# Kernel optimization log

Hardware: AMD Instinct MI355X
Metric: run time of the kernel (lower is better)

## Reference

```python
import jax, jax.numpy as jnp
import numpy as np

N = 50000      # nodes
E = 800000     # edges (before self-loops)
F_IN = 767     # input feature dim
HID = 256      # hidden = 8 heads * 32
NEG_SLOPE = 0.2


def setup_inputs() -> dict:
    key = jax.random.key(0)
    ks = jax.random.split(key, 10)
    x = jax.random.normal(ks[0], (N, F_IN), dtype=jnp.float32)
    edge_index = jax.random.randint(ks[1], (2, E), 0, N, dtype=jnp.int64)
    # GATConv 1: 767 -> 8 heads x 32 (concat -> 256)
    W1 = jax.random.normal(ks[2], (F_IN, HID), dtype=jnp.float32) * 0.05
    att_src1 = jax.random.normal(ks[3], (8, 32), dtype=jnp.float32) * 0.1
    att_dst1 = jax.random.normal(ks[4], (8, 32), dtype=jnp.float32) * 0.1
    b1 = jnp.zeros((HID,), dtype=jnp.float32)
    # GATConv 2: 256 -> 1 head x 10 (mean -> 10)
    W2 = jax.random.normal(ks[5], (HID, 10), dtype=jnp.float32) * 0.05
    att_src2 = jax.random.normal(ks[6], (1, 10), dtype=jnp.float32) * 0.1
    att_dst2 = jax.random.normal(ks[7], (1, 10), dtype=jnp.float32) * 0.1
    b2 = jnp.zeros((10,), dtype=jnp.float32)
    return {"x": x, "edge_index": edge_index, "W1": W1, "att_src1": att_src1,
            "att_dst1": att_dst1, "b1": b1, "W2": W2, "att_src2": att_src2,
            "att_dst2": att_dst2, "b2": b2}


def _gat_conv(x, src, dst, W, att_s, att_d, b, heads, ch, concat):
    """PyG GATConv (eval mode, dropout inactive). x:[N,Fin], src/dst:[E']."""
    n = x.shape[0]
    h = (x @ W).reshape(n, heads, ch)                      # [N,H,C]
    a_s = jnp.sum(h * att_s, axis=-1)                      # [N,H]
    a_d = jnp.sum(h * att_d, axis=-1)                      # [N,H]
    e = jax.nn.leaky_relu(a_s[src] + a_d[dst], NEG_SLOPE)  # [E',H]
    # destination-grouped (segment) softmax, numerically stable
    m = jax.lax.stop_gradient(jax.ops.segment_max(e, dst, num_segments=n))
    p = jnp.exp(e - m[dst])                                # [E',H]
    denom = jax.ops.segment_sum(p, dst, num_segments=n)    # [N,H]
    alpha = p / (denom[dst] + 1e-16)                       # [E',H]
    # scatter-aggregate weighted messages
    out = jax.ops.segment_sum(alpha[:, :, None] * h[src], dst, num_segments=n)
    out = out.reshape(n, heads * ch) if concat else out.mean(axis=1)
    return out + b


def reference(x, edge_index, W1, att_src1, att_dst1, b1, W2, att_src2, att_dst2, b2):
    n = x.shape[0]
    loops = jnp.arange(n, dtype=edge_index.dtype)
    src = jnp.concatenate([edge_index[0], loops])
    dst = jnp.concatenate([edge_index[1], loops])
    h = jax.nn.elu(_gat_conv(x, src, dst, W1, att_src1, att_dst1, b1, 8, 32, True))
    # dropout is a no-op in eval mode
    return _gat_conv(h, src, dst, W2, att_src2, att_dst2, b2, 1, 10, False)
```

## Files before the change

kernel.cpp:

```cpp
#include <hip/hip_runtime.h>
#include <hip/hip_fp16.h>

#define N_NODES 50000
#define N_EDGES 800000
#define EL (N_EDGES + N_NODES)
#define F_IN 767
#define HID 256
#define NHEAD 8
#define KSTEPS 24
#define NCH 12
#define NB_SCAN 49

typedef __attribute__((ext_vector_type(8))) short short8;
typedef __attribute__((ext_vector_type(4))) float f32x4;

struct H4 { __half2 a, b; };

static __device__ __forceinline__ unsigned short f2bf(float f) {
  unsigned int u = __float_as_uint(f);
  unsigned int r = (u + 0x7fffu + ((u >> 16) & 1u)) >> 16;
  return (unsigned short)r;
}
static __device__ __forceinline__ float bf2f(unsigned short h) {
  return __uint_as_float(((unsigned int)h) << 16);
}

__global__ __launch_bounds__(256) void prep_kernel(
    const float* __restrict__ W, short* __restrict__ Wh, short* __restrict__ Wl) {
  int idx = blockIdx.x * 256 + threadIdx.x;
  int k = idx >> 8, n = idx & 255;
  float v = (k < F_IN) ? W[k * HID + n] : 0.f;
  unsigned short h = f2bf(v);
  float lf = v - bf2f(h);
  unsigned short lo = f2bf(lf);
  int ks = k >> 5, oct = (k >> 3) & 3, j = k & 7;
  int nf = n >> 4;
  int l = (n & 15) | (oct << 4);
  int addr = ((ks * 16 + nf) * 64 + l) * 8 + j;
  Wh[addr] = (short)h;
  Wl[addr] = (short)lo;
}

__global__ __launch_bounds__(256, 2) void gemm1_mfma_kernel(
    const float* __restrict__ x, const short* __restrict__ Wh,
    const short* __restrict__ Wl, __half* __restrict__ h1h,
    const float* __restrict__ att_s, const float* __restrict__ att_d,
    float* __restrict__ as1, float* __restrict__ ad1) {
  __shared__ __align__(16) short Ah[2][2][2048];
  const int tid = threadIdx.x;
  const int lane = tid & 63, wav = tid >> 6;
  const int m0 = blockIdx.x * 64;
  const int m_local = tid >> 2, oct = tid & 3;
  const int gm = m0 + m_local;
  const bool vrow = (gm < N_NODES);
  const long xbase = (long)gm * F_IN;
  const int wu0 = ((m_local >> 4) * 64) + ((m_local & 15) | (oct << 4));
  const int wu = wu0 ^ ((((unsigned)wu0 >> 4) & 3) << 1);

  float atts[4], attd[4];
#pragma unroll
  for (int nf = 0; nf < 4; ++nf) {
    int c = wav * 64 + nf * 16 + (lane & 15);
    atts[nf] = att_s[c];
    attd[nf] = att_d[c];
  }

  f32x4 acc[4][4];
#pragma unroll
  for (int i = 0; i < 4; ++i)
#pragma unroll
    for (int j = 0; j < 4; ++j) acc[i][j] = (f32x4){0.f, 0.f, 0.f, 0.f};

  float xc[16], xn[16];
  {
    int kb = oct * 8;
    if (vrow) {
#pragma unroll
      for (int ki = 0; ki < 2; ++ki)
#pragma unroll
        for (int j = 0; j < 8; ++j) {
          xc[ki * 8 + j] = x[xbase + kb + ki * 32 + j];
          xn[ki * 8 + j] = x[xbase + 64 + kb + ki * 32 + j];
        }
    } else {
#pragma unroll
      for (int j = 0; j < 16; ++j) { xc[j] = 0.f; xn[j] = 0.f; }
    }
  }
  short8 bhc[4], blc[4];
  {
    const short* wb = Wh + ((wav * 4) * 64 + lane) * 8;
    const short* wbl = Wl + ((wav * 4) * 64 + lane) * 8;
#pragma unroll
    for (int nf = 0; nf < 4; ++nf) {
      bhc[nf] = *(const short8*)(wb + nf * 512);
      blc[nf] = *(const short8*)(wbl + nf * 512);
    }
  }

#pragma unroll 2
  for (int c = 0; c < NCH; ++c) {
#pragma unroll
    for (int ki = 0; ki < 2; ++ki) {
      short8 hi8;
#pragma unroll
      for (int j = 0; j < 8; ++j) hi8[j] = (short)f2bf(xc[ki * 8 + j]);
      *(short8*)&Ah[c & 1][ki][wu * 8] = hi8;
    }
    {
#pragma unroll
      for (int j = 0; j < 16; ++j) xc[j] = xn[j];
      int s = c + 2;
      if (s < NCH - 1) {
        int kb = s * 64 + oct * 8;
        if (vrow) {
#pragma unroll
          for (int ki = 0; ki < 2; ++ki)
#pragma unroll
            for (int j = 0; j < 8; ++j) xn[ki * 8 + j] = x[xbase + kb + ki * 32 + j];
        } else {
#pragma unroll
          for (int j = 0; j < 16; ++j) xn[j] = 0.f;
        }
      } else if (s == NCH - 1) {
        int kb = s * 64 + oct * 8;
#pragma unroll
        for (int ki = 0; ki < 2; ++ki)
#pragma unroll
          for (int j = 0; j < 8; ++j) {
            int k = kb + ki * 32 + j;
            xn[ki * 8 + j] = (vrow && k < F_IN) ? x[xbase + k] : 0.f;
          }
      }
    }
    __syncthreads();
#pragma unroll
    for (int ki = 0; ki < 2; ++ki) {
      const int ksg = c * 2 + ki;
      short8 ah[4];
#pragma unroll
      for (int mf = 0; mf < 4; ++mf) {
        int u = mf * 64 + lane;
        int us = u ^ ((((unsigned)u >> 4) & 3) << 1);
        ah[mf] = *(short8*)&Ah[c & 1][ki][us * 8];
      }
      short8 bhn[4], bln[4];
      if (ksg + 1 < KSTEPS) {
        const short* wb = Wh + (((ksg + 1) * 16 + wav * 4) * 64 + lane) * 8;
        const short* wbl = Wl + (((ksg + 1) * 16 + wav * 4) * 64 + lane) * 8;
#pragma unroll
        for (int nf = 0; nf < 4; ++nf) {
          bhn[nf] = *(const short8*)(wb + nf * 512);
          bln[nf] = *(const short8*)(wbl + nf * 512);
        }
      }
#pragma unroll
      for (int mf = 0; mf < 4; ++mf)
#pragma unroll
        for (int nf = 0; nf < 4; ++nf)
          acc[mf][nf] = __builtin_amdgcn_mfma_f32_16x16x32_bf16(ah[mf], bhc[nf], acc[mf][nf], 0, 0, 0);
#pragma unroll
      for (int mf = 0; mf < 4; ++mf)
#pragma unroll
        for (int nf = 0; nf < 4; ++nf)
          acc[mf][nf] = __builtin_amdgcn_mfma_f32_16x16x32_bf16(ah[mf], blc[nf], acc[mf][nf], 0, 0, 0);
#pragma unroll
      for (int nf = 0; nf < 4; ++nf) {
        bhc[nf] = bhn[nf];
        blc[nf] = bln[nf];
      }
    }
  }

  const int r0 = (lane >> 4) * 4, cn = lane & 15;
#pragma unroll
  for (int mf = 0; mf < 4; ++mf) {
    int rowb = m0 + mf * 16 + r0;
#pragma unroll
    for (int rr = 0; rr < 4; ++rr) {
      int row = rowb + rr;
      bool ok = (row < N_NODES);
      if (ok) {
#pragma unroll
        for (int nf = 0; nf < 4; ++nf)
          h1h[(long)row * HID + wav * 64 + nf * 16 + cn] =
              __float2half_rn(acc[mf][nf][rr]);
      }
      float s0 = acc[mf][0][rr] * atts[0] + acc[mf][1][rr] * atts[1];
      float s1 = acc[mf][2][rr] * atts[2] + acc[mf][3][rr] * atts[3];
      float d0 = acc[mf][0][rr] * attd[0] + acc[mf][1][rr] * attd[1];
      float d1 = acc[mf][2][rr] * attd[2] + acc[mf][3][rr] * attd[3];
#pragma unroll
      for (int o = 1; o < 16; o <<= 1) {
        s0 += __shfl_xor(s0, o, 64);
        s1 += __shfl_xor(s1, o, 64);
        d0 += __shfl_xor(d0, o, 64);
        d1 += __shfl_xor(d1, o, 64);
      }
      if (ok && cn == 0) {
        as1[row * NHEAD + wav * 2]     = s0;
        as1[row * NHEAD + wav * 2 + 1] = s1;
        ad1[row * NHEAD + wav * 2]     = d0;
        ad1[row * NHEAD + wav * 2 + 1] = d1;
      }
    }
  }
}

__global__ void count_kernel(const int* __restrict__ ei, int* __restrict__ deg) {
  int e = blockIdx.x * blockDim.x + threadIdx.x;
  if (e >= EL) return;
  int dst = (e < N_EDGES) ? ei[N_EDGES + e] : (e - N_EDGES);
  atomicAdd(&deg[dst], 1);
}

__global__ __launch_bounds__(1024) void scan_part_kernel(
    const int* __restrict__ deg, int* __restrict__ off, int* __restrict__ btot) {
  __shared__ int warp_sums[16];
  const int tid = threadIdx.x;
  const int lane = tid & 63, wid = tid >> 6;
  int i = blockIdx.x * 1024 + tid;
  int v = (i < N_NODES) ? deg[i] : 0;
  int x = v;
#pragma unroll
  for (int o = 1; o < 64; o <<= 1) {
    int y = __shfl_up(x, o, 64);
    if (lane >= o) x += y;
  }
  if (lane == 63) warp_sums[wid] = x;
  __syncthreads();
  if (wid == 0) {
    int ws = (lane < 16) ? warp_sums[lane] : 0;
#pragma unroll
    for (int o = 1; o < 16; o <<= 1) {
      int y = __shfl_up(ws, o, 64);
      if (lane >= o) ws += y;
    }
    if (lane < 16) warp_sums[lane] = ws;
  }
  __syncthreads();
  int wprefix = (wid > 0) ? warp_sums[wid - 1] : 0;
  if (i < N_NODES) off[i] = wprefix + x - v;
  if (tid == 1023) btot[blockIdx.x] = warp_sums[15];
}

__global__ __launch_bounds__(64) void scan_tops_kernel(
    const int* __restrict__ btot, int* __restrict__ bo) {
  int lane = threadIdx.x;
  int v = (lane < NB_SCAN) ? btot[lane] : 0;
  int x = v;
#pragma unroll
  for (int o = 1; o < 64; o <<= 1) {
    int y = __shfl_up(x, o, 64);
    if (lane >= o) x += y;
  }
  if (lane < NB_SCAN) bo[lane] = x - v;
}

__global__ void scan_add_kernel(int* __restrict__ off, const int* __restrict__ bo) {
  int i = blockIdx.x * blockDim.x + threadIdx.x;
  if (i > N_NODES) return;
  if (i == N_NODES) off[i] = EL;
  else off[i] += bo[i >> 10];
}

__global__ void fill_kernel(const int* __restrict__ ei, const int* __restrict__ off,
                            int* __restrict__ cur, int* __restrict__ csr) {
  int e = blockIdx.x * blockDim.x + threadIdx.x;
  if (e >= EL) return;
  int src, dst;
  if (e < N_EDGES) { src = ei[e]; dst = ei[N_EDGES + e]; }
  else { src = e - N_EDGES; dst = src; }
  int pos = atomicAdd(&cur[dst], 1);
  csr[off[dst] + pos] = src;
}

__global__ __launch_bounds__(256) void agg1_kernel(
    const __half* __restrict__ h1h, const float* __restrict__ as1,
    const float* __restrict__ ad1, const int* __restrict__ off,
    const int* __restrict__ csr, const float* __restrict__ b1,
    const float* __restrict__ W2, const float* __restrict__ att_s2,
    const float* __restrict__ att_d2, float* __restrict__ h2,
    float* __restrict__ as2, float* __restrict__ ad2) {
  __shared__ float W2s[HID * 11];
  {
    int tid = threadIdx.x;
    for (int i = tid; i < HID * 10; i += 256)
      W2s[(i / 10) * 11 + (i % 10)] = W2[i];
  }
  __syncthreads();
  const int t = threadIdx.x & 63;
  const int n = blockIdx.x * 4 + (threadIdx.x >> 6);
  if (n >= N_NODES) return;
  const int head = t >> 3;
  const float adn = ad1[n * NHEAD + head];
  const int j0 = off[n], j1 = off[n + 1];
  float a0 = 0.f, a1 = 0.f, a2 = 0.f, a3 = 0.f, den = 0.f;
  int j = j0;
  for (; j + 3 < j1; j += 4) {
    int s[4];
    float pw[4];
    H4 v[4];
#pragma unroll
    for (int q = 0; q < 4; ++q) s[q] = csr[j + q];
#pragma unroll
    for (int q = 0; q < 4; ++q) {
      float e = as1[s[q] * NHEAD + head] + adn;
      e = (e >= 0.f) ? e : 0.2f * e;
      pw[q] = __expf(e);
      v[q] = *(const H4*)&h1h[s[q] * HID + t * 4];
    }
#pragma unroll
    for (int q = 0; q < 4; ++q) {
      float2 fa = __half22float2(v[q].a), fb = __half22float2(v[q].b);
      den += pw[q];
      a0 += pw[q] * fa.x;
      a1 += pw[q] * fa.y;
      a2 += pw[q] * fb.x;
      a3 += pw[q] * fb.y;
    }
  }
  for (; j < j1; ++j) {
    int s0 = csr[j];
    float e = as1[s0 * NHEAD + head] + adn;
    e = (e >= 0.f) ? e : 0.2f * e;
    float p0 = __expf(e);
    H4 v0 = *(const H4*)&h1h[s0 * HID + t * 4];
    float2 fa = __half22float2(v0.a), fb = __half22float2(v0.b);
    den += p0;
    a0 += p0 * fa.x;
    a1 += p0 * fa.y;
    a2 += p0 * fb.x;
    a3 += p0 * fb.y;
  }
  float rden = 1.f / (den + 1e-16f);
  float4 bv = *(const float4*)&b1[t * 4];
  float vv[4];
  vv[0] = a0 * rden + bv.x;
  vv[1] = a1 * rden + bv.y;
  vv[2] = a2 * rden + bv.z;
  vv[3] = a3 * rden + bv.w;
#pragma unroll
  for (int c = 0; c < 4; ++c) vv[c] = (vv[c] > 0.f) ? vv[c] : (__expf(vv[c]) - 1.f);
  float hk[10];
#pragma unroll
  for (int k = 0; k < 10; ++k) {
    float pk = vv[0] * W2s[(t * 4 + 0) * 11 + k] +
               vv[1] * W2s[(t * 4 + 1) * 11 + k] +
               vv[2] * W2s[(t * 4 + 2) * 11 + k] +
               vv[3] * W2s[(t * 4 + 3) * 11 + k];
#pragma unroll
    for (int o = 32; o >= 1; o >>= 1) pk += __shfl_xor(pk, o, 64);
    hk[k] = pk;
  }
  if (t == 0) {
    float s = 0.f, d = 0.f;
#pragma unroll
    for (int k = 0; k < 10; ++k) {
      h2[n * 10 + k] = hk[k];
      s += hk[k] * att_s2[k];
      d += hk[k] * att_d2[k];
    }
    as2[n] = s;
    ad2[n] = d;
  }
}

__global__ __launch_bounds__(256) void agg2_kernel(
    const float* __restrict__ h2, const float* __restrict__ as2,
    const float* __restrict__ ad2, const int* __restrict__ off,
    const int* __restrict__ csr, const float* __restrict__ b2,
    float* __restrict__ out) {
  int g = threadIdx.x >> 4, l = threadIdx.x & 15;
  int n = blockIdx.x * 16 + g;
  if (n >= N_NODES) return;
  float adn = ad2[n];
  int j0 = off[n], j1 = off[n + 1];
  float acc = 0.f, den = 0.f;
  int j = j0;
  for (; j + 1 < j1; j += 2) {
    int s0 = csr[j], s1 = csr[j + 1];
    float e0 = as2[s0] + adn, e1 = as2[s1] + adn;
    e0 = (e0 >= 0.f) ? e0 : 0.2f * e0;
    e1 = (e1 >= 0.f) ? e1 : 0.2f * e1;
    float p0 = __expf(e0), p1v = __expf(e1);
    den += p0 + p1v;
    if (l < 10) acc += p0 * h2[s0 * 10 + l] + p1v * h2[s1 * 10 + l];
  }
  if (j < j1) {
    int s0 = csr[j];
    float e0 = as2[s0] + adn;
    e0 = (e0 >= 0.f) ? e0 : 0.2f * e0;
    float p0 = __expf(e0);
    den += p0;
    if (l < 10) acc += p0 * h2[s0 * 10 + l];
  }
  if (l < 10) out[n * 10 + l] = acc / (den + 1e-16f) + b2[l];
}

extern "C" void kernel_launch(void* const* d_in, const int* in_sizes, int n_in,
                              void* d_out, int out_size, void* d_ws, size_t ws_size,
                              hipStream_t stream) {
  const float* x    = (const float*)d_in[0];
  const int*   ei   = (const int*)d_in[1];
  const float* W1   = (const float*)d_in[2];
  const float* as1w = (const float*)d_in[3];
  const float* ad1w = (const float*)d_in[4];
  const float* b1   = (const float*)d_in[5];
  const float* W2   = (const float*)d_in[6];
  const float* as2w = (const float*)d_in[7];
  const float* ad2w = (const float*)d_in[8];
  const float* b2   = (const float*)d_in[9];
  float* out = (float*)d_out;

  char* p = (char*)d_ws;
  __half* h1h = (__half*)p; p += (size_t)N_NODES * HID * 2;
  float* a_s1 = (float*)p; p += (size_t)N_NODES * NHEAD * 4;
  float* a_d1 = (float*)p; p += (size_t)N_NODES * NHEAD * 4;
  float* h2   = (float*)p; p += (size_t)N_NODES * 10 * 4;
  float* a_s2 = (float*)p; p += (size_t)N_NODES * 4;
  float* a_d2 = (float*)p; p += (size_t)N_NODES * 4;
  short* Wh   = (short*)p; p += (size_t)KSTEPS * 16 * 64 * 8 * 2;
  short* Wl   = (short*)p; p += (size_t)KSTEPS * 16 * 64 * 8 * 2;
  int* deg    = (int*)p;   p += (size_t)N_NODES * 4;
  int* cur    = (int*)p;   p += (size_t)N_NODES * 4;
  int* off    = (int*)p;   p += (size_t)(N_NODES + 1) * 4;
  int* csr    = (int*)p;   p += (size_t)EL * 4;
  int* btot   = (int*)p;   p += 64 * 4;
  int* bo     = (int*)p;   p += 64 * 4;

  prep_kernel<<<768, 256, 0, stream>>>(W1, Wh, Wl);
  gemm1_mfma_kernel<<<(N_NODES + 63) / 64, 256, 0, stream>>>(
      x, Wh, Wl, h1h, as1w, ad1w, a_s1, a_d1);
  hipMemsetAsync(deg, 0, (size_t)N_NODES * 2 * 4, stream);
  count_kernel<<<(EL + 255) / 256, 256, 0, stream>>>(ei, deg);
  scan_part_kernel<<<NB_SCAN, 1024, 0, stream>>>(deg, off, btot);
  scan_tops_kernel<<<1, 64, 0, stream>>>(btot, bo);
  scan_add_kernel<<<(N_NODES + 256) / 256, 256, 0, stream>>>(off, bo);
  fill_kernel<<<(EL + 255) / 256, 256, 0, stream>>>(ei, off, cur, csr);
  agg1_kernel<<<(N_NODES + 3) / 4, 256, 0, stream>>>(
      h1h, a_s1, a_d1, off, csr, b1, W2, as2w, ad2w, h2, a_s2, a_d2);
  agg2_kernel<<<(N_NODES + 15) / 16, 256, 0, stream>>>(h2, a_s2, a_d2, off, csr, b2, out);
}
```

Measured before the change: 282.5 us.

## Load GEMM A fragments directly from global memory, removing LDS staging and barriers

The first-layer GEMM no longer stages converted x tiles through shared memory with a per-chunk __syncthreads. Each wave now loads its own A fragments straight from global memory in MFMA operand layout, converts them to bf16 in registers, and prefetches two k-steps ahead with double-buffered register arrays. This removes the LDS traffic and block barriers. In exchange, every one of the four waves redundantly loads the same x rows (4x global/L2 reads of A), and the per-lane loads are strided 8-float reads rather than the previous shared cooperative layout.

```diff
diff --git a/kernel.cpp b/kernel.cpp
--- a/kernel.cpp
+++ b/kernel.cpp
@@ -8,7 +8,6 @@
 #define HID 256
 #define NHEAD 8
 #define KSTEPS 24
-#define NCH 12
 #define NB_SCAN 49
 
 typedef __attribute__((ext_vector_type(8))) short short8;
@@ -46,21 +45,23 @@
     const short* __restrict__ Wl, __half* __restrict__ h1h,
     const float* __restrict__ att_s, const float* __restrict__ att_d,
     float* __restrict__ as1, float* __restrict__ ad1) {
-  __shared__ __align__(16) short Ah[2][2][2048];
   const int tid = threadIdx.x;
   const int lane = tid & 63, wav = tid >> 6;
   const int m0 = blockIdx.x * 64;
-  const int m_local = tid >> 2, oct = tid & 3;
-  const int gm = m0 + m_local;
-  const bool vrow = (gm < N_NODES);
-  const long xbase = (long)gm * F_IN;
-  const int wu0 = ((m_local >> 4) * 64) + ((m_local & 15) | (oct << 4));
-  const int wu = wu0 ^ ((((unsigned)wu0 >> 4) & 3) << 1);
+  const int fr = lane & 15, oct = lane >> 4;
+  long abase[4];
+  bool vr[4];
+#pragma unroll
+  for (int mf = 0; mf < 4; ++mf) {
+    int r = m0 + mf * 16 + fr;
+    vr[mf] = (r < N_NODES);
+    abase[mf] = (long)r * F_IN + oct * 8;
+  }
 
   float atts[4], attd[4];
 #pragma unroll
   for (int nf = 0; nf < 4; ++nf) {
-    int c = wav * 64 + nf * 16 + (lane & 15);
+    int c = wav * 64 + nf * 16 + fr;
     atts[nf] = att_s[c];
     attd[nf] = att_d[c];
   }
@@ -71,20 +72,17 @@
 #pragma unroll
     for (int j = 0; j < 4; ++j) acc[i][j] = (f32x4){0.f, 0.f, 0.f, 0.f};
 
-  float xc[16], xn[16];
-  {
-    int kb = oct * 8;
-    if (vrow) {
-#pragma unroll
-      for (int ki = 0; ki < 2; ++ki)
-#pragma unroll
-        for (int j = 0; j < 8; ++j) {
-          xc[ki * 8 + j] = x[xbase + kb + ki * 32 + j];
-          xn[ki * 8 + j] = x[xbase + 64 + kb + ki * 32 + j];
-        }
+  float xa0[4][8], xa1[4][8];
+#pragma unroll
+  for (int mf = 0; mf < 4; ++mf) {
+    if (vr[mf]) {
+#pragma unroll
+      for (int j = 0; j < 8; ++j) xa0[mf][j] = x[abase[mf] + j];
+#pragma unroll
+      for (int j = 0; j < 8; ++j) xa1[mf][j] = x[abase[mf] + 32 + j];
     } else {
 #pragma unroll
-      for (int j = 0; j < 16; ++j) { xc[j] = 0.f; xn[j] = 0.f; }
+      for (int j = 0; j < 8; ++j) { xa0[mf][j] = 0.f; xa1[mf][j] = 0.f; }
     }
   }
   short8 bhc[4], blc[4];
@@ -98,78 +96,62 @@
     }
   }
 
-#pragma unroll 2
-  for (int c = 0; c < NCH; ++c) {
-#pragma unroll
-    for (int ki = 0; ki < 2; ++ki) {
-      short8 hi8;
-#pragma unroll
-      for (int j = 0; j < 8; ++j) hi8[j] = (short)f2bf(xc[ki * 8 + j]);
-      *(short8*)&Ah[c & 1][ki][wu * 8] = hi8;
-    }
-    {
-#pragma unroll
-      for (int j = 0; j < 16; ++j) xc[j] = xn[j];
-      int s = c + 2;
-      if (s < NCH - 1) {
-        int kb = s * 64 + oct * 8;
-        if (vrow) {
-#pragma unroll
-          for (int ki = 0; ki < 2; ++ki)
-#pragma unroll
-            for (int j = 0; j < 8; ++j) xn[ki * 8 + j] = x[xbase + kb + ki * 32 + j];
-        } else {
-#pragma unroll
-          for (int j = 0; j < 16; ++j) xn[j] = 0.f;
-        }
-      } else if (s == NCH - 1) {
-        int kb = s * 64 + oct * 8;
-#pragma unroll
-        for (int ki = 0; ki < 2; ++ki)
-#pragma unroll
-          for (int j = 0; j < 8; ++j) {
-            int k = kb + ki * 32 + j;
-            xn[ki * 8 + j] = (vrow && k < F_IN) ? x[xbase + k] : 0.f;
-          }
-      }
-    }
-    __syncthreads();
-#pragma unroll
-    for (int ki = 0; ki < 2; ++ki) {
-      const int ksg = c * 2 + ki;
-      short8 ah[4];
+  auto step = [&](int ks, float (&cur)[4][8]) {
+    short8 ah[4];
+#pragma unroll
+    for (int mf = 0; mf < 4; ++mf)
+#pragma unroll
+      for (int j = 0; j < 8; ++j) ah[mf][j] = (short)f2bf(cur[mf][j]);
+    int s = ks + 2;
+    if (s < KSTEPS - 1) {
+      int kb = s * 32;
 #pragma unroll
       for (int mf = 0; mf < 4; ++mf) {
-        int u = mf * 64 + lane;
-        int us = u ^ ((((unsigned)u >> 4) & 3) << 1);
-        ah[mf] = *(short8*)&Ah[c & 1][ki][us * 8];
-      }
-      short8 bhn[4], bln[4];
-      if (ksg + 1 < KSTEPS) {
-        const short* wb = Wh + (((ksg + 1) * 16 + wav * 4) * 64 + lane) * 8;
-        const short* wbl = Wl + (((ksg + 1) * 16 + wav * 4) * 64 + lane) * 8;
-#pragma unroll
-        for (int nf = 0; nf < 4; ++nf) {
-          bhn[nf] = *(const short8*)(wb + nf * 512);
-          bln[nf] = *(const short8*)(wbl + nf * 512);
+        if (vr[mf]) {
+#pragma unroll
+          for (int j = 0; j < 8; ++j) cur[mf][j] = x[abase[mf] + kb + j];
         }
       }
+    } else if (s == KSTEPS - 1) {
+      int kb = s * 32;
 #pragma unroll
       for (int mf = 0; mf < 4; ++mf)
 #pragma unroll
-        for (int nf = 0; nf < 4; ++nf)
-          acc[mf][nf] = __builtin_amdgcn_mfma_f32_16x16x32_bf16(ah[mf], bhc[nf], acc[mf][nf], 0, 0, 0);
-#pragma unroll
-      for (int mf = 0; mf < 4; ++mf)
-#pragma unroll
-        for (int nf = 0; nf < 4; ++nf)
-          acc[mf][nf] = __builtin_amdgcn_mfma_f32_16x16x32_bf16(ah[mf], blc[nf], acc[mf][nf], 0, 0, 0);
+        for (int j = 0; j < 8; ++j) {
+          int k = kb + oct * 8 + j;
+          cur[mf][j] = (vr[mf] && k < F_IN) ? x[abase[mf] + kb + j] : 0.f;
+        }
+    }
+    short8 bhn[4], bln[4];
+    if (ks + 1 < KSTEPS) {
+      const short* wb = Wh + (((ks + 1) * 16 + wav * 4) * 64 + lane) * 8;
+      const short* wbl = Wl + (((ks + 1) * 16 + wav * 4) * 64 + lane) * 8;
 #pragma unroll
       for (int nf = 0; nf < 4; ++nf) {
-        bhc[nf] = bhn[nf];
-        blc[nf] = bln[nf];
+        bhn[nf] = *(const short8*)(wb + nf * 512);
+        bln[nf] = *(const short8*)(wbl + nf * 512);
       }
     }
+#pragma unroll
+    for (int mf = 0; mf < 4; ++mf)
+#pragma unroll
+      for (int nf = 0; nf < 4; ++nf)
+        acc[mf][nf] = __builtin_amdgcn_mfma_f32_16x16x32_bf16(ah[mf], bhc[nf], acc[mf][nf], 0, 0, 0);
+#pragma unroll
+    for (int mf = 0; mf < 4; ++mf)
+#pragma unroll
+      for (int nf = 0; nf < 4; ++nf)
+        acc[mf][nf] = __builtin_amdgcn_mfma_f32_16x16x32_bf16(ah[mf], blc[nf], acc[mf][nf], 0, 0, 0);
+#pragma unroll
+    for (int nf = 0; nf < 4; ++nf) {
+      bhc[nf] = bhn[nf];
+      blc[nf] = bln[nf];
+    }
+  };
+
+  for (int kp = 0; kp < KSTEPS / 2; ++kp) {
+    step(2 * kp, xa0);
+    step(2 * kp + 1, xa1);
   }
 
   const int r0 = (lane >> 4) * 4, cn = lane & 15;
```

After: 366.3 us. +29.6%, slower.
